# Kernel optimization log

Hardware: AMD Instinct MI355X
Metric: run time of the kernel (lower is better)

The kernel has to match this reference:

```python
import jax, jax.numpy as jnp
import numpy as np

B = 16; L_IN = 512; D_MODEL = 512; N_HEAD = 8; D_K = 128; D_V = 128
D_FF = 2048; N_LAYER = 4; WINDOW = (4, 4, 4); INNER = 5; COV = 4; NUM_SEQ = 128
N_LVL = len(WINDOW) + 1


def _build_mask_sizes():
    # Pyraformer get_mask: intra-scale band + inter-scale parent/child links.
    all_size = [L_IN]
    for w in WINDOW:
        all_size.append(all_size[-1] // w)
    L = sum(all_size)
    vis = np.zeros((L, L), dtype=bool)
    iw = INNER // 2
    starts = [0]
    for s in all_size:
        starts.append(starts[-1] + s)
    for li, sz in enumerate(all_size):
        s = starts[li]
        for i in range(s, s + sz):
            vis[i, max(i - iw, s):min(i + iw + 1, s + sz)] = True
    for li in range(1, len(all_size)):
        s = starts[li]
        for i in range(s, s + all_size[li]):
            l = (s - all_size[li - 1]) + (i - s) * WINDOW[li - 1]
            if i == s + all_size[li] - 1:
                r = s
            else:
                r = (s - all_size[li - 1]) + (i - s + 1) * WINDOW[li - 1]
            vis[i, l:r] = True
            vis[l:r, i] = True
    return ~vis, all_size  # True = blocked


def _build_indexes(all_size):
    # Pyraformer refer_points: for each fine position, its ancestor at each scale.
    idx = np.zeros((L_IN, len(all_size)), dtype=np.int64)
    for i in range(L_IN):
        idx[i, 0] = i
        former = i
        for j in range(1, len(all_size)):
            start = sum(all_size[:j])
            inner = former - (start - all_size[j - 1])
            former = start + min(inner // WINDOW[j - 1], all_size[j] - 1)
            idx[i, j] = former
    return idx


def _layer_norm(x, g, b, eps=1e-5):
    m = x.mean(-1, keepdims=True)
    v = x.var(-1, keepdims=True)
    return (x - m) / jnp.sqrt(v + eps) * g + b


def _conv1d(x, w, stride):  # x: [B,C,L], w: [O,I,K]
    return jax.lax.conv_general_dilated(x, w, (stride,), 'VALID',
                                        dimension_numbers=('NCH', 'OIH', 'NCH'))


def _forward(x, cov_w, cov_b, data_conv_w, down_w, down_b, conv_w, conv_b, bn_g, bn_b,
             up_w, up_b, bln_g, bln_b, wq, wk, wv, fc_w, ln1_g, ln1_b,
             ffn_w1, ffn_b1, ffn_w2, ffn_b2, ln2_g, ln2_b, attn_mask, gather_idx):
    Bsz = x.shape[0]
    # SingleStepEmbedding
    covs = jnp.concatenate([x[:, :, 1:1 + COV], (x[:, :, -1] / NUM_SEQ - 0.5)[..., None]], -1)
    cov_emb = covs @ cov_w + cov_b
    data = x[:, :, 0][:, None, :]                      # [B,1,L]
    data = jnp.concatenate([data[:, :, -1:], data, data[:, :, :1]], -1)  # circular pad k=3
    data_emb = _conv1d(data, data_conv_w, 1).transpose(0, 2, 1)          # [B,L,D]
    i = jnp.arange(D_MODEL)
    vec = jnp.power(10000.0, 2.0 * (i // 2) / D_MODEL)
    ang = jnp.arange(L_IN)[:, None] / vec
    pos_emb = jnp.where(i % 2 == 0, jnp.sin(ang), jnp.cos(ang))
    seq = cov_emb + data_emb + pos_emb[None]
    # Bottleneck_Construct (down -> strided convs -> up -> concat -> LN)
    tmp = (seq @ down_w + down_b).transpose(0, 2, 1)   # [B,d_k,L]
    outs = []
    for s in range(len(WINDOW)):
        tmp = _conv1d(tmp, conv_w[s], WINDOW[s]) + conv_b[s][None, :, None]
        mu = tmp.mean((0, 2), keepdims=True)
        var = tmp.var((0, 2), keepdims=True)
        tmp = (tmp - mu) / jnp.sqrt(var + 1e-5) * bn_g[s][None, :, None] + bn_b[s][None, :, None]
        tmp = jax.nn.elu(tmp)
        outs.append(tmp)
    pyr = jnp.concatenate(outs, axis=2).transpose(0, 2, 1) @ up_w + up_b
    enc = _layer_norm(jnp.concatenate([seq, pyr], axis=1), bln_g, bln_b)  # [B,Ltot,D]
    Lt = enc.shape[1]
    scale = np.float32(1.0 / np.sqrt(D_K))
    for l in range(N_LAYER):
        q = (enc @ wq[l]).reshape(Bsz, Lt, N_HEAD, D_K).transpose(0, 2, 1, 3)
        k = (enc @ wk[l]).reshape(Bsz, Lt, N_HEAD, D_K).transpose(0, 2, 1, 3)
        v = (enc @ wv[l]).reshape(Bsz, Lt, N_HEAD, D_V).transpose(0, 2, 1, 3)
        scores = jnp.einsum('bhqd,bhkd->bhqk', q, k) * scale
        scores = jnp.where(attn_mask[None, None], -1e9, scores)
        attn = jax.nn.softmax(scores, -1)
        o = jnp.einsum('bhqk,bhkd->bhqd', attn, v).transpose(0, 2, 1, 3).reshape(Bsz, Lt, N_HEAD * D_V)
        enc = _layer_norm(o @ fc_w[l] + enc, ln1_g[l], ln1_b[l])  # post-norm
        h = jax.nn.gelu(enc @ ffn_w1[l] + ffn_b1[l], approximate=False) @ ffn_w2[l] + ffn_b2[l]
        enc = _layer_norm(enc + h, ln2_g[l], ln2_b[l])
    # refer_points gather: [B, L_IN, N_LVL*D]
    out = enc[:, gather_idx.reshape(-1), :].reshape(Bsz, L_IN, N_LVL * D_MODEL)
    return out


def setup_inputs() -> dict:
    key = jax.random.key(0)
    ks = iter(jax.random.split(key, 64))

    def nrm(shape, scale=0.02):
        return (jax.random.normal(next(ks), shape) * scale).astype(jnp.float32)

    covs = jax.random.normal(next(ks), (B, L_IN, COV + 1), jnp.float32)
    ids = jax.random.randint(next(ks), (B, L_IN), 0, NUM_SEQ).astype(jnp.float32)
    x = jnp.concatenate([covs, ids[..., None]], -1)  # col0=data, 1..COV=covs, last=series id
    mask_np, all_size = _build_mask_sizes()
    idx = _build_indexes(all_size)
    nw = len(WINDOW)
    return dict(
        x=x,
        cov_w=nrm((COV + 1, D_MODEL)), cov_b=jnp.zeros((D_MODEL,), jnp.float32),
        data_conv_w=nrm((D_MODEL, 1, 3)),
        down_w=nrm((D_MODEL, D_K)), down_b=jnp.zeros((D_K,), jnp.float32),
        conv_w=nrm((nw, D_K, D_K, WINDOW[0])), conv_b=jnp.zeros((nw, D_K), jnp.float32),
        bn_g=jnp.ones((nw, D_K), jnp.float32), bn_b=jnp.zeros((nw, D_K), jnp.float32),
        up_w=nrm((D_K, D_MODEL)), up_b=jnp.zeros((D_MODEL,), jnp.float32),
        bln_g=jnp.ones((D_MODEL,), jnp.float32), bln_b=jnp.zeros((D_MODEL,), jnp.float32),
        wq=nrm((N_LAYER, D_MODEL, N_HEAD * D_K)), wk=nrm((N_LAYER, D_MODEL, N_HEAD * D_K)),
        wv=nrm((N_LAYER, D_MODEL, N_HEAD * D_V)), fc_w=nrm((N_LAYER, N_HEAD * D_V, D_MODEL)),
        ln1_g=jnp.ones((N_LAYER, D_MODEL), jnp.float32), ln1_b=jnp.zeros((N_LAYER, D_MODEL), jnp.float32),
        ffn_w1=nrm((N_LAYER, D_MODEL, D_FF)), ffn_b1=jnp.zeros((N_LAYER, D_FF), jnp.float32),
        ffn_w2=nrm((N_LAYER, D_FF, D_MODEL)), ffn_b2=jnp.zeros((N_LAYER, D_MODEL), jnp.float32),
        ln2_g=jnp.ones((N_LAYER, D_MODEL), jnp.float32), ln2_b=jnp.zeros((N_LAYER, D_MODEL), jnp.float32),
        attn_mask=jnp.asarray(mask_np),
        gather_idx=jnp.asarray(idx),
    )


def reference(x, cov_w, cov_b, data_conv_w, down_w, down_b, conv_w, conv_b, bn_g, bn_b,
              up_w, up_b, bln_g, bln_b, wq, wk, wv, fc_w, ln1_g, ln1_b,
              ffn_w1, ffn_b1, ffn_w2, ffn_b2, ln2_g, ln2_b, attn_mask, gather_idx):
    return _forward(x, cov_w, cov_b, data_conv_w, down_w, down_b, conv_w, conv_b, bn_g, bn_b,
                    up_w, up_b, bln_g, bln_b, wq, wk, wv, fc_w, ln1_g, ln1_b,
                    ffn_w1, ffn_b1, ffn_w2, ffn_b2, ln2_g, ln2_b, attn_mask, gather_idx)
```

## Files before the change

kernel.cpp:

```cpp
#include <hip/hip_runtime.h>
#include <math.h>

typedef unsigned short u16;
typedef unsigned int u32;
typedef __attribute__((ext_vector_type(8))) short s16x8;
typedef __attribute__((ext_vector_type(4))) float f32x4;
typedef __attribute__((ext_vector_type(4))) u32 u32x4;
typedef __attribute__((ext_vector_type(2))) u32 u32x2;

#define LT 680

static __device__ __forceinline__ float bf2f(u16 u) {
  u32 v = ((u32)u) << 16;
  return __builtin_bit_cast(float, v);
}
static __device__ __forceinline__ u16 f2bf(float f) {
  u32 u = __builtin_bit_cast(u32, f);
  u32 r = (u + 0x7FFFu + ((u >> 16) & 1u)) >> 16;
  return (u16)r;
}
static __device__ __forceinline__ float lo16(u32 u) {
  return __builtin_bit_cast(float, u << 16);
}
static __device__ __forceinline__ float hi16(u32 u) {
  return __builtin_bit_cast(float, u & 0xFFFF0000u);
}

static __device__ __forceinline__ void gload16(const u16* g, u16* l) {
  __builtin_amdgcn_global_load_lds(
      (const __attribute__((address_space(1))) u32*)g,
      (__attribute__((address_space(3))) u32*)l, 16, 0, 0);
}

__global__ void detect_k(const u32* __restrict__ blng, int* __restrict__ flag) {
  if (threadIdx.x == 0 && blockIdx.x == 0)
    *flag = (blng[0] == 0x3F803F80u) ? 1 : 0;
}

struct CvtArgs {
  const void* src[20];
  float* dst[20];
  int pre[21];
};

__global__ __launch_bounds__(256) void cvtall_k(CvtArgs a, const int* __restrict__ flag) {
  int i = blockIdx.x * 256 + threadIdx.x;
  if (i >= a.pre[20]) return;
  int s = 0;
#pragma unroll
  for (int k = 1; k <= 20; ++k)
    if (i >= a.pre[k]) s = k;
  int j = i - a.pre[s];
  bool isb = (*flag != 0);
  a.dst[s][j] = isb ? bf2f(((const u16*)a.src[s])[j]) : ((const float*)a.src[s])[j];
}

__global__ __launch_bounds__(256) void tc2_k(const void* __restrict__ S,
                                             u16* __restrict__ D, int K, int N,
                                             size_t sstride, size_t dstride,
                                             const int* __restrict__ flag) {
  __shared__ u16 t[32][33];
  size_t soff = (size_t)blockIdx.z * sstride;
  D += (size_t)blockIdx.z * dstride;
  int nb = blockIdx.x * 32, kb = blockIdx.y * 32;
  int lx = threadIdx.x & 31, ly = threadIdx.x >> 5;
  bool isb = (*flag != 0);
#pragma unroll
  for (int i = 0; i < 4; ++i) {
    size_t idx = soff + (size_t)(kb + ly + 8 * i) * N + nb + lx;
    t[ly + 8 * i][lx] = isb ? ((const u16*)S)[idx] : f2bf(((const float*)S)[idx]);
  }
  __syncthreads();
#pragma unroll
  for (int i = 0; i < 4; ++i)
    D[(size_t)(nb + ly + 8 * i) * K + kb + lx] = t[lx][ly + 8 * i];
}

static __device__ __forceinline__ void reduce2_256(float& a, float& b, float* sm) {
#pragma unroll
  for (int o = 32; o; o >>= 1) { a += __shfl_xor(a, o); b += __shfl_xor(b, o); }
  int w = threadIdx.x >> 6, ln = threadIdx.x & 63;
  if (ln == 0) { sm[w] = a; sm[4 + w] = b; }
  __syncthreads();
  a = sm[0] + sm[1] + sm[2] + sm[3];
  b = sm[4] + sm[5] + sm[6] + sm[7];
  __syncthreads();
}

__global__ __launch_bounds__(256) void emb_k(
    const float* __restrict__ x, const float* __restrict__ covw,
    const float* __restrict__ covb, const float* __restrict__ dw,
    float* __restrict__ seq) {
  int r = blockIdx.x;
  int b = r >> 9, l = r & 511;
  int base = r * 6;
  float c0 = x[base + 1], c1 = x[base + 2];
  float c2 = x[base + 3], c3 = x[base + 4];
  float c4 = x[base + 5] * 0.0078125f - 0.5f;
  int lm = (l + 511) & 511, lp = (l + 1) & 511;
  float dm = x[((b << 9) + lm) * 6];
  float d0 = x[base];
  float dp = x[((b << 9) + lp) * 6];
  for (int d = threadIdx.x; d < 512; d += 256) {
    float cov = c0 * covw[d] + c1 * covw[512 + d] +
                c2 * covw[1024 + d] + c3 * covw[1536 + d] +
                c4 * covw[2048 + d] + covb[d];
    float cv = dm * dw[d * 3] + d0 * dw[d * 3 + 1] + dp * dw[d * 3 + 2];
    float ex = (float)(2 * (d >> 1)) * (1.0f / 512.0f);
    float vec = powf(10000.0f, ex);
    float ang = (float)l / vec;
    float pos = (d & 1) ? cosf(ang) : sinf(ang);
    seq[((size_t)r << 9) + d] = cov + cv + pos;
  }
}

__global__ void tconv_k(const float* __restrict__ w, float* __restrict__ wt) {
  int e = blockIdx.x * 256 + threadIdx.x;
  if (e >= 3 * 512 * 128) return;
  int o = e & 127, ik = (e >> 7) & 511, s = e >> 16;
  wt[e] = w[s * 65536 + o * 512 + ik];
}

__global__ __launch_bounds__(256) void gemm_k(
    const float* __restrict__ A, const float* __restrict__ Bw,
    const float* __restrict__ bias, float* __restrict__ C,
    int M, int N, int K, int act) {
  __shared__ float As[16][64];
  __shared__ float Bs[16][64];
  int tid = threadIdx.x;
  int m0 = blockIdx.y * 64, n0 = blockIdx.x * 64;
  int tx = tid & 15, ty = tid >> 4;
  int la_r = tid >> 2, la_c = (tid & 3) << 2;
  int lb_r = tid >> 4, lb_c = (tid & 15) << 2;
  float acc[4][4] = {};
  for (int k0 = 0; k0 < K; k0 += 16) {
    float4 av = *reinterpret_cast<const float4*>(A + (size_t)(m0 + la_r) * K + k0 + la_c);
    As[la_c + 0][la_r] = av.x;
    As[la_c + 1][la_r] = av.y;
    As[la_c + 2][la_r] = av.z;
    As[la_c + 3][la_r] = av.w;
    float4 bv = *reinterpret_cast<const float4*>(Bw + (size_t)(k0 + lb_r) * N + n0 + lb_c);
    Bs[lb_r][lb_c + 0] = bv.x;
    Bs[lb_r][lb_c + 1] = bv.y;
    Bs[lb_r][lb_c + 2] = bv.z;
    Bs[lb_r][lb_c + 3] = bv.w;
    __syncthreads();
#pragma unroll
    for (int kk = 0; kk < 16; ++kk) {
      float4 a4 = *reinterpret_cast<const float4*>(&As[kk][ty << 2]);
      float4 b4 = *reinterpret_cast<const float4*>(&Bs[kk][tx << 2]);
      float ar[4] = {a4.x, a4.y, a4.z, a4.w};
      float br[4] = {b4.x, b4.y, b4.z, b4.w};
#pragma unroll
      for (int i = 0; i < 4; ++i)
#pragma unroll
        for (int j = 0; j < 4; ++j) acc[i][j] = fmaf(ar[i], br[j], acc[i][j]);
    }
    __syncthreads();
  }
  float bj[4] = {0.f, 0.f, 0.f, 0.f};
  if (bias) {
#pragma unroll
    for (int j = 0; j < 4; ++j) bj[j] = bias[n0 + (tx << 2) + j];
  }
#pragma unroll
  for (int i = 0; i < 4; ++i) {
    float4 o;
    float* op = reinterpret_cast<float*>(&o);
#pragma unroll
    for (int j = 0; j < 4; ++j) op[j] = acc[i][j] + bj[j];
    *reinterpret_cast<float4*>(C + (size_t)(m0 + (ty << 2) + i) * N + n0 + (tx << 2)) = o;
  }
}

static __device__ __forceinline__ f32x4 mfma16(s16x8 a, s16x8 b, f32x4 c) {
  return __builtin_amdgcn_mfma_f32_16x16x32_bf16(a, b, c, 0, 0, 0);
}

__global__ __launch_bounds__(256) void mgemm_k(
    const u16* __restrict__ A, const u16* __restrict__ BT,
    const float* __restrict__ bias, void* __restrict__ C,
    int M, int N, int K, int flags) {
  __shared__ char smem[49152];
  float* st = (float*)smem;
  int tid = threadIdx.x;

  int nN = N >> 7;
  int nwg = gridDim.x;
  int bid = blockIdx.x;
  int qq = nwg >> 3, rr = nwg & 7;
  int xcd = bid & 7, lin = bid >> 3;
  int s_ = (xcd < rr ? xcd * (qq + 1) : rr * (qq + 1) + (xcd - rr) * qq) + lin;
  int m0 = (s_ / nN) << 7, n0 = (s_ % nN) << 7;

  int l = tid & 63, wid = tid >> 6;
  int wr = wid >> 1, wc = wid & 1;
  f32x4 acc[4][4];
#pragma unroll
  for (int i = 0; i < 4; ++i)
#pragma unroll
    for (int j = 0; j < 4; ++j)
#pragma unroll
      for (int r = 0; r < 4; ++r) acc[i][j][r] = 0.f;

  int L8 = l >> 3;
  int p0_ = (l & 7) ^ L8;
  int rloc = 2 * L8 + (p0_ >> 2);
  int cel = (p0_ & 3) << 3;
  const u16* Ag0 = A + (size_t)m0 * K;
  const u16* Bg0 = BT + (size_t)n0 * K;

  auto STAGE = [&](int c, int kt) {
    u16* Ad = (u16*)smem + c * 8192;
    u16* Bd = Ad + 4096;
#pragma unroll
    for (int i = 0; i < 2; ++i) {
      int rg = wid * 32 + i * 16 + rloc;
      gload16(Ag0 + (size_t)rg * K + kt + cel, &Ad[(wid * 16 + i * 8) * 64]);
      gload16(Bg0 + (size_t)rg * K + kt + cel, &Bd[(wid * 16 + i * 8) * 64]);
    }
  };

  int sfrag = (((l & 1) << 2) + (l >> 4)) ^ (((l & 15) >> 1));
  int lhalf = (l & 15) >> 1;

  int nt = K >> 5;
  STAGE(0, 0);
  STAGE(1, 32);
  for (int t = 0; t < nt; ++t) {
    int cur = t % 3;
    if (t + 2 < nt) {
      STAGE((t + 2) % 3, (t + 2) << 5);
      asm volatile("s_waitcnt vmcnt(8)" ::: "memory");
    } else if (t + 1 < nt) {
      asm volatile("s_waitcnt vmcnt(4)" ::: "memory");
    } else {
      asm volatile("s_waitcnt vmcnt(0)" ::: "memory");
    }
    __builtin_amdgcn_s_barrier();
    const u16* Asb = (const u16*)smem + cur * 8192;
    const u16* Bsb = Asb + 4096;
    s16x8 af[4];
#pragma unroll
    for (int fr = 0; fr < 4; ++fr)
      af[fr] = *reinterpret_cast<const s16x8*>(
          &Asb[(wr * 32 + fr * 8 + lhalf) * 64 + sfrag * 8]);
#pragma unroll
    for (int fc = 0; fc < 4; ++fc) {
      s16x8 bf = *reinterpret_cast<const s16x8*>(
          &Bsb[(wc * 32 + fc * 8 + lhalf) * 64 + sfrag * 8]);
#pragma unroll
      for (int fr = 0; fr < 4; ++fr)
        acc[fr][fc] = mfma16(af[fr], bf, acc[fr][fc]);
    }
    asm volatile("s_waitcnt lgkmcnt(0)" ::: "memory");
    __builtin_amdgcn_s_barrier();
  }

  int cl = l & 15, rg2 = l >> 4;
  float bj[4];
#pragma unroll
  for (int fc = 0; fc < 4; ++fc)
    bj[fc] = bias ? bias[n0 + wc * 64 + fc * 16 + cl] : 0.f;
  int sr2 = tid >> 3;
  int scg = (tid & 7) << 4;
  int growb = m0 + ((sr2 >> 4) << 6) + (sr2 & 15);
#pragma unroll
  for (int fr = 0; fr < 4; ++fr) {
#pragma unroll
    for (int fc = 0; fc < 4; ++fc) {
      int col = wc * 64 + fc * 16 + cl;
#pragma unroll
      for (int r = 0; r < 4; ++r) {
        float v = acc[fr][fc][r] + bj[fc];
        if (flags & 2) {
          float zz = 1.5957691f * fmaf(0.044715f * v, v * v, v);
          v = v / (1.0f + __expf(-zz));
        }
        st[(wr * 16 + rg2 * 4 + r) * 132 + col] = v;
      }
    }
    __syncthreads();
    int gr = growb + fr * 16;
    if (flags & 1) {
      u32x4 o0, o1;
      u16* p0 = (u16*)&o0; u16* p1 = (u16*)&o1;
#pragma unroll
      for (int i = 0; i < 8; ++i) p0[i] = f2bf(st[sr2 * 132 + scg + i]);
#pragma unroll
      for (int i = 0; i < 8; ++i) p1[i] = f2bf(st[sr2 * 132 + scg + 8 + i]);
      u16* dst = (u16*)C + (size_t)gr * N + n0 + scg;
      __builtin_nontemporal_store(o0, reinterpret_cast<u32x4*>(dst));
      __builtin_nontemporal_store(o1, reinterpret_cast<u32x4*>(dst + 8));
    } else {
      float* dst = (float*)C + (size_t)gr * N + n0 + scg;
#pragma unroll
      for (int i = 0; i < 4; ++i)
        __builtin_nontemporal_store(
            *reinterpret_cast<const f32x4*>(&st[sr2 * 132 + scg + 4 * i]),
            reinterpret_cast<f32x4*>(dst + 4 * i));
    }
    __syncthreads();
  }
}

__global__ __launch_bounds__(256) void mg64_k(
    const u16* __restrict__ A, const u16* __restrict__ BT,
    const float* __restrict__ bias, float* __restrict__ C,
    int M, int N, int K) {
  __shared__ char smem[49152];
  float* st = (float*)smem;
  int tid = threadIdx.x;

  int nN = N >> 6;
  int nwg = gridDim.x;
  int bid = blockIdx.x;
  int qq = nwg >> 3, rr = nwg & 7;
  int xcd = bid & 7, lin = bid >> 3;
  int s_ = (xcd < rr ? xcd * (qq + 1) : rr * (qq + 1) + (xcd - rr) * qq) + lin;
  int m0 = (s_ / nN) << 6, n0 = (s_ % nN) << 6;

  int l = tid & 63, wid = tid >> 6;
  f32x4 acc[4];
#pragma unroll
  for (int j = 0; j < 4; ++j)
#pragma unroll
    for (int r = 0; r < 4; ++r) acc[j][r] = 0.f;

  int row8 = l >> 3, cp = l & 7;
  int cg = (cp ^ (row8 & 7)) << 3;
  const u16* Ag0 = A + (size_t)m0 * K;
  const u16* Bg0 = BT + (size_t)n0 * K;

  auto STAGE = [&](int c, int kt) {
    u16* Ad = (u16*)smem + c * 8192;
    u16* Bd = Ad + 4096;
#pragma unroll
    for (int i = 0; i < 2; ++i) {
      int r = wid * 16 + i * 8 + row8;
      gload16(Ag0 + (size_t)r * K + kt + cg, &Ad[(wid * 16 + i * 8) * 64]);
      gload16(Bg0 + (size_t)r * K + kt + cg, &Bd[(wid * 16 + i * 8) * 64]);
    }
  };

  int nt = K >> 6;
  STAGE(0, 0);
  STAGE(1, 64);
  for (int t = 0; t < nt; ++t) {
    int cur = t % 3;
    if (t + 2 < nt) {
      STAGE((t + 2) % 3, (t + 2) << 6);
      asm volatile("s_waitcnt vmcnt(8)" ::: "memory");
    } else if (t + 1 < nt) {
      asm volatile("s_waitcnt vmcnt(4)" ::: "memory");
    } else {
      asm volatile("s_waitcnt vmcnt(0)" ::: "memory");
    }
    __builtin_amdgcn_s_barrier();
    const u16* Asb = (const u16*)smem + cur * 8192;
    const u16* Bsb = Asb + 4096;
#pragma unroll
    for (int kk = 0; kk < 2; ++kk) {
      int kc = ((kk * 4 + (l >> 4)) ^ (l & 7)) * 8;
      s16x8 af = *reinterpret_cast<const s16x8*>(
          &Asb[(wid * 16 + (l & 15)) * 64 + kc]);
#pragma unroll
      for (int fc = 0; fc < 4; ++fc) {
        s16x8 bf = *reinterpret_cast<const s16x8*>(
            &Bsb[(fc * 16 + (l & 15)) * 64 + kc]);
        acc[fc] = mfma16(af, bf, acc[fc]);
      }
    }
    asm volatile("s_waitcnt lgkmcnt(0)" ::: "memory");
    __builtin_amdgcn_s_barrier();
  }

  int cl = l & 15, rg = l >> 4;
  float bj[4];
#pragma unroll
  for (int fc = 0; fc < 4; ++fc)
    bj[fc] = bias ? bias[n0 + fc * 16 + cl] : 0.f;
#pragma unroll
  for (int fc = 0; fc < 4; ++fc)
#pragma unroll
    for (int r = 0; r < 4; ++r)
      st[(wid * 16 + rg * 4 + r) * 80 + fc * 16 + cl] = acc[fc][r] + bj[fc];
  __syncthreads();
  int lr = tid >> 2;
  int lq = (tid & 3) << 2;
  float* dst = C + (size_t)(m0 + lr) * N + n0;
#pragma unroll
  for (int i = 0; i < 4; ++i)
    __builtin_nontemporal_store(
        *reinterpret_cast<const f32x4*>(&st[lr * 80 + lq + 16 * i]),
        reinterpret_cast<f32x4*>(dst + lq + 16 * i));
}

__global__ void im2col_k(const float* __restrict__ Y, float* __restrict__ X,
                         int Ti, int To) {
  int e = blockIdx.x * 256 + threadIdx.x;
  int ik = e & 511;
  int bt = e >> 9;
  int b = bt / To, t = bt - b * To;
  int i = ik >> 2, k = ik & 3;
  X[e] = Y[((size_t)(b * Ti + (t << 2) + k) << 7) + i];
}

__global__ __launch_bounds__(256) void bnelu_k(float* __restrict__ Y,
                                               const float* __restrict__ g,
                                               const float* __restrict__ be, int Ms) {
  __shared__ float sm[8];
  int ch = blockIdx.x;
  float s = 0.f, s2 = 0.f;
  for (int i = threadIdx.x; i < Ms; i += 256) {
    float v = Y[((size_t)i << 7) + ch];
    s += v; s2 += v * v;
  }
  reduce2_256(s, s2, sm);
  float mu = s / (float)Ms;
  float var = s2 / (float)Ms - mu * mu;
  float inv = rsqrtf(var + 1e-5f);
  float ga = g[ch], bb = be[ch];
  for (int i = threadIdx.x; i < Ms; i += 256) {
    float v = (Y[((size_t)i << 7) + ch] - mu) * inv * ga + bb;
    Y[((size_t)i << 7) + ch] = (v > 0.f) ? v : (expf(v) - 1.0f);
  }
}

__global__ void scat_k(const float* __restrict__ Y, float* __restrict__ cat,
                       int Ts, int off) {
  int e = blockIdx.x * 256 + threadIdx.x;
  int i = e & 127;
  int bt = e >> 7;
  int b = bt / Ts, t = bt - b * Ts;
  cat[((size_t)(b * 168 + off + t) << 7) + i] = Y[e];
}

__global__ __launch_bounds__(256) void catln_k(
    const float* __restrict__ seq, const float* __restrict__ pyr,
    const float* __restrict__ g, const float* __restrict__ be,
    float* __restrict__ out, u16* __restrict__ outb) {
  __shared__ float sm[8];
  int row = blockIdx.x;
  int b = row / LT, j = row - b * LT;
  const float* src = (j < 512) ? (seq + ((size_t)(b * 512 + j) << 9))
                               : (pyr + ((size_t)(b * 168 + j - 512) << 9));
  int t = threadIdx.x;
  float x0 = src[t], x1 = src[t + 256];
  float s = x0 + x1, s2 = x0 * x0 + x1 * x1;
  reduce2_256(s, s2, sm);
  float mu = s * 0.001953125f;
  float var = s2 * 0.001953125f - mu * mu;
  float inv = rsqrtf(var + 1e-5f);
  size_t ob = (size_t)row << 9;
  float v0 = (x0 - mu) * inv * g[t] + be[t];
  float v1 = (x1 - mu) * inv * g[t + 256] + be[t + 256];
  out[ob + t] = v0; out[ob + t + 256] = v1;
  outb[ob + t] = f2bf(v0); outb[ob + t + 256] = f2bf(v1);
}

__global__ __launch_bounds__(256) void lnres_k(
    const float* __restrict__ A, const float* __restrict__ R,
    const float* __restrict__ g, const float* __restrict__ be,
    float* __restrict__ O, u16* __restrict__ Ob) {
  __shared__ float sm[8];
  int row = blockIdx.x;
  size_t base = (size_t)row << 9;
  int t = threadIdx.x;
  float x0 = A[base + t] + R[base + t];
  float x1 = A[base + t + 256] + R[base + t + 256];
  float s = x0 + x1, s2 = x0 * x0 + x1 * x1;
  reduce2_256(s, s2, sm);
  float mu = s * 0.001953125f;
  float var = s2 * 0.001953125f - mu * mu;
  float inv = rsqrtf(var + 1e-5f);
  float v0 = (x0 - mu) * inv * g[t] + be[t];
  float v1 = (x1 - mu) * inv * g[t + 256] + be[t + 256];
  O[base + t] = v0; O[base + t + 256] = v1;
  Ob[base + t] = f2bf(v0); Ob[base + t + 256] = f2bf(v1);
}

__global__ __launch_bounds__(256) void attn_k(const u16* __restrict__ QKV,
                                              u16* __restrict__ O) {
  int cpx = gridDim.x >> 3;
  int bq = (blockIdx.x & 7) * cpx + (blockIdx.x >> 3);
  int b = bq / LT, q = bq - b * LT;
  int lane = threadIdx.x & 63, wv = threadIdx.x >> 6;
  int half = lane >> 5, t4 = (lane & 31) << 2;
  int h = (wv << 1) + half;
  int lvl = (q < 512) ? 0 : (q < 640) ? 1 : (q < 672) ? 2 : 3;
  int Sl = (lvl == 0) ? 0 : (lvl == 1) ? 512 : (lvl == 2) ? 640 : 672;
  int SZl = (lvl == 0) ? 512 : (lvl == 1) ? 128 : (lvl == 2) ? 32 : 8;
  int p = q - Sl;
  int Sc = (lvl == 1) ? 0 : (lvl == 2) ? 512 : 640;
  int Sp = (lvl == 0) ? 512 : (lvl == 1) ? 640 : 672;
  int tg[10];
  bool vd[10];
#pragma unroll
  for (int jj = 0; jj < 10; ++jj) {
    int tgt; bool valid;
    if (jj < 5) { int pp = p - 2 + jj; valid = (pp >= 0 && pp < SZl); tgt = Sl + pp; }
    else if (jj < 9) { valid = (lvl > 0); tgt = Sc + p * 4 + (jj - 5); }
    else { valid = (lvl < 3); tgt = Sp + (p >> 2); }
    if (!valid) tgt = q;
    tg[jj] = tgt; vd[jj] = valid;
  }
  size_t hoff = h * 128 + t4;
  u32x2 qv = *reinterpret_cast<const u32x2*>(QKV + (size_t)bq * 3072 + hoff);
  float q0 = lo16(qv.x), q1 = hi16(qv.x), q2 = lo16(qv.y), q3 = hi16(qv.y);
  size_t base3 = (size_t)b * LT;
  float sc[10];
  float mx = -1e30f;
#pragma unroll
  for (int jj = 0; jj < 10; ++jj) {
    u32x2 kv = *reinterpret_cast<const u32x2*>(
        QKV + (base3 + tg[jj]) * 3072 + 1024 + hoff);
    float pr = q0 * lo16(kv.x) + q1 * hi16(kv.x) + q2 * lo16(kv.y) + q3 * hi16(kv.y);
#pragma unroll
    for (int o = 16; o; o >>= 1) pr += __shfl_xor(pr, o);
    float sv = vd[jj] ? pr * 0.08838834764831845f : -1e30f;
    sc[jj] = sv;
    mx = fmaxf(mx, sv);
  }
  float den = 0.f;
#pragma unroll
  for (int jj = 0; jj < 10; ++jj) { sc[jj] = expf(sc[jj] - mx); den += sc[jj]; }
  float invd = 1.0f / den;
  float o0 = 0.f, o1 = 0.f, o2 = 0.f, o3 = 0.f;
#pragma unroll
  for (int jj = 0; jj < 10; ++jj) {
    u32x2 vv = *reinterpret_cast<const u32x2*>(
        QKV + (base3 + tg[jj]) * 3072 + 2048 + hoff);
    float w = sc[jj] * invd;
    o0 = fmaf(w, lo16(vv.x), o0);
    o1 = fmaf(w, hi16(vv.x), o1);
    o2 = fmaf(w, lo16(vv.y), o2);
    o3 = fmaf(w, hi16(vv.y), o3);
  }
  u32x2 ov;
  ov.x = (u32)f2bf(o0) | ((u32)f2bf(o1) << 16);
  ov.y = (u32)f2bf(o2) | ((u32)f2bf(o3) << 16);
  *reinterpret_cast<u32x2*>(O + (size_t)bq * 1024 + hoff) = ov;
}

__global__ void gather_k(const float* __restrict__ enc, void* __restrict__ out,
                         const int* __restrict__ flag) {
  int e = blockIdx.x * 256 + threadIdx.x;
  int d = e & 511;
  int lvl = (e >> 9) & 3;
  int i = (e >> 11) & 511;
  int b = e >> 20;
  int g = (lvl == 0) ? i
        : (lvl == 1) ? (512 + (i >> 2))
        : (lvl == 2) ? (640 + (i >> 4))
                     : (672 + (i >> 6));
  float v = enc[(((size_t)b * LT + g) << 9) + d];
  if (*flag) ((u16*)out)[e] = f2bf(v);
  else       ((float*)out)[e] = v;
}

extern "C" void kernel_launch(void* const* d_in, const int* in_sizes, int n_in,
                              void* d_out, int out_size, void* d_ws, size_t ws_size,
                              hipStream_t stream) {
  float* ws = (float*)d_ws;
  size_t off = 0;
  auto alloc = [&](size_t n) { float* p = ws + off; off += (n + 63) & ~(size_t)63; return p; };

  int* flag = (int*)alloc(64);

  static const int cvt_n[26] = {
      49152, 2560, 512, 1536, 65536, 128, 196608, 384, 384, 384,
      65536, 512, 512, 512, 2097152, 2097152, 2097152, 2097152, 2048, 2048,
      4194304, 8192, 4194304, 2048, 2048, 2048};
  float* cf[26];
  for (int i = 0; i < 26; ++i) cf[i] = alloc(cvt_n[i]);

  float* cwt     = alloc(196608);
  float* enc     = alloc((size_t)10880 * 512);
  float* tmp     = alloc((size_t)10880 * 512);
  u16*   encb    = (u16*)alloc((size_t)10880 * 512 / 2);
  u16*   qkv     = (u16*)alloc((size_t)10880 * 3072 / 2);
  u16*   attnout = (u16*)alloc((size_t)10880 * 1024 / 2);
  u16*   qkvw    = (u16*)alloc((size_t)4 * 3072 * 512 / 2);
  u16*   fcT     = (u16*)alloc((size_t)4 * 512 * 1024 / 2);
  u16*   w1T     = (u16*)alloc((size_t)4 * 2048 * 512 / 2);
  u16*   w2T     = (u16*)alloc((size_t)4 * 512 * 2048 / 2);
  u16*   H1      = qkv;

  float* seq   = (float*)qkv;
  float* pyr   = seq + 4194304;
  float* tdown = pyr + 1376256;
  float* xcol  = tdown + 1048576;
  float* ya    = xcol + 1048576;
  float* yb    = ya + 262144;
  float* yc    = yb + 65536;
  float* cat   = yc + 16384;

  detect_k<<<1, 64, 0, stream>>>((const u32*)d_in[12], flag);
  {
    static const int segs[20] = {0,1,2,3,4,5,6,7,8,9,10,11,12,13,18,19,21,23,24,25};
    CvtArgs a;
    int acc_ = 0;
    for (int k = 0; k < 20; ++k) {
      int i = segs[k];
      a.src[k] = d_in[i];
      a.dst[k] = cf[i];
      a.pre[k] = acc_;
      acc_ += cvt_n[i];
    }
    a.pre[20] = acc_;
    cvtall_k<<<(acc_ + 255) / 256, 256, 0, stream>>>(a, flag);
  }

  const float *x = cf[0], *covw = cf[1], *covb = cf[2], *dconvw = cf[3],
              *downw = cf[4], *downb = cf[5], *convw = cf[6], *convb = cf[7],
              *bng = cf[8], *bnb = cf[9], *upw = cf[10], *upb = cf[11],
              *blng = cf[12], *blnb = cf[13], *ln1g = cf[18], *ln1b = cf[19],
              *b1 = cf[21], *b2 = cf[23], *ln2g = cf[24], *ln2b = cf[25];

  tc2_k<<<dim3(32, 16, 4), 256, 0, stream>>>(d_in[14], qkvw,           512, 1024, 524288, 1572864, flag);
  tc2_k<<<dim3(32, 16, 4), 256, 0, stream>>>(d_in[15], qkvw + 524288,  512, 1024, 524288, 1572864, flag);
  tc2_k<<<dim3(32, 16, 4), 256, 0, stream>>>(d_in[16], qkvw + 1048576, 512, 1024, 524288, 1572864, flag);
  tc2_k<<<dim3(16, 32, 4), 256, 0, stream>>>(d_in[17], fcT,  1024, 512, 524288, 524288, flag);
  tc2_k<<<dim3(64, 16, 4), 256, 0, stream>>>(d_in[20], w1T,  512, 2048, 1048576, 1048576, flag);
  tc2_k<<<dim3(16, 64, 4), 256, 0, stream>>>(d_in[22], w2T,  2048, 512, 1048576, 1048576, flag);

  emb_k<<<8192, 256, 0, stream>>>(x, covw, covb, dconvw, seq);
  tconv_k<<<(3 * 512 * 128 + 255) / 256, 256, 0, stream>>>(convw, cwt);

  gemm_k<<<dim3(2, 128), 256, 0, stream>>>(seq, downw, downb, tdown, 8192, 128, 512, 0);
  im2col_k<<<(16 * 128 * 512) / 256, 256, 0, stream>>>(tdown, xcol, 512, 128);
  gemm_k<<<dim3(2, 32), 256, 0, stream>>>(xcol, cwt, convb, ya, 2048, 128, 512, 0);
  bnelu_k<<<128, 256, 0, stream>>>(ya, bng, bnb, 2048);
  scat_k<<<(2048 * 128) / 256, 256, 0, stream>>>(ya, cat, 128, 0);
  im2col_k<<<(16 * 32 * 512) / 256, 256, 0, stream>>>(ya, xcol, 128, 32);
  gemm_k<<<dim3(2, 8), 256, 0, stream>>>(xcol, cwt + 65536, convb + 128, yb, 512, 128, 512, 0);
  bnelu_k<<<128, 256, 0, stream>>>(yb, bng + 128, bnb + 128, 512);
  scat_k<<<(512 * 128) / 256, 256, 0, stream>>>(yb, cat, 32, 128);
  im2col_k<<<(16 * 8 * 512) / 256, 256, 0, stream>>>(yb, xcol, 32, 8);
  gemm_k<<<dim3(2, 2), 256, 0, stream>>>(xcol, cwt + 131072, convb + 256, yc, 128, 128, 512, 0);
  bnelu_k<<<128, 256, 0, stream>>>(yc, bng + 256, bnb + 256, 128);
  scat_k<<<(128 * 128) / 256, 256, 0, stream>>>(yc, cat, 8, 160);
  gemm_k<<<dim3(8, 42), 256, 0, stream>>>(cat, upw, upb, pyr, 2688, 512, 128, 0);
  catln_k<<<10880, 256, 0, stream>>>(seq, pyr, blng, blnb, enc, encb);

  for (int l = 0; l < 4; ++l) {
    const u16* qw  = qkvw + (size_t)l * 3072 * 512;
    const u16* fw  = fcT + (size_t)l * 524288;
    const u16* w1w = w1T + (size_t)l * 1048576;
    const u16* w2w = w2T + (size_t)l * 1048576;
    mgemm_k<<<85 * 24, 256, 0, stream>>>(encb, qw, nullptr, qkv, 10880, 3072, 512, 1);
    attn_k<<<16 * LT, 256, 0, stream>>>(qkv, attnout);
    mg64_k<<<170 * 8, 256, 0, stream>>>(attnout, fw, nullptr, tmp, 10880, 512, 1024);
    lnres_k<<<10880, 256, 0, stream>>>(tmp, enc, ln1g + l * 512, ln1b + l * 512, enc, encb);
    mgemm_k<<<85 * 16, 256, 0, stream>>>(encb, w1w, b1 + l * 2048, H1, 10880, 2048, 512, 3);
    mg64_k<<<170 * 8, 256, 0, stream>>>(H1, w2w, b2 + l * 512, tmp, 10880, 512, 2048);
    lnres_k<<<10880, 256, 0, stream>>>(tmp, enc, ln2g + l * 512, ln2b + l * 512, enc, encb);
  }

  gather_k<<<(16 * 512 * 2048) / 256, 256, 0, stream>>>(enc, d_out, flag);
}
```

Baseline: 1.228 ms.

## Split-K the N=512 output-projection GEMMs and fuse partial sums into layernorm

The fc and FFN-down GEMMs (N=512, K=1024/2048) now run as split-K with two halves, doubling the workgroup count to 2720 so the GPU is better occupied. Each half writes fp32 partials to a separate buffer, and the residual layernorm kernel sums both partials plus the bias. In exchange, each GEMM writes twice as much fp32 output and the layernorm reads one extra activation-sized tensor. Some unused converted-weight buffers are also dropped from the workspace to make room.

```diff
diff --git a/kernel.cpp b/kernel.cpp
--- a/kernel.cpp
+++ b/kernel.cpp
@@ -304,17 +304,20 @@
   }
 }
 
-__global__ __launch_bounds__(256) void mg64_k(
+__global__ __launch_bounds__(256) void mg64sk_k(
     const u16* __restrict__ A, const u16* __restrict__ BT,
-    const float* __restrict__ bias, float* __restrict__ C,
-    int M, int N, int K) {
+    float* __restrict__ C, int M, int N, int K, int Ksub) {
   __shared__ char smem[49152];
   float* st = (float*)smem;
   int tid = threadIdx.x;
 
+  int half = blockIdx.x & 1;
+  int bid = blockIdx.x >> 1;
+  int koff = half * Ksub;
+  C += (size_t)half * M * N;
+
   int nN = N >> 6;
-  int nwg = gridDim.x;
-  int bid = blockIdx.x;
+  int nwg = gridDim.x >> 1;
   int qq = nwg >> 3, rr = nwg & 7;
   int xcd = bid & 7, lin = bid >> 3;
   int s_ = (xcd < rr ? xcd * (qq + 1) : rr * (qq + 1) + (xcd - rr) * qq) + lin;
@@ -329,8 +332,8 @@
 
   int row8 = l >> 3, cp = l & 7;
   int cg = (cp ^ (row8 & 7)) << 3;
-  const u16* Ag0 = A + (size_t)m0 * K;
-  const u16* Bg0 = BT + (size_t)n0 * K;
+  const u16* Ag0 = A + (size_t)m0 * K + koff;
+  const u16* Bg0 = BT + (size_t)n0 * K + koff;
 
   auto STAGE = [&](int c, int kt) {
     u16* Ad = (u16*)smem + c * 8192;
@@ -343,7 +346,7 @@
     }
   };
 
-  int nt = K >> 6;
+  int nt = Ksub >> 6;
   STAGE(0, 0);
   STAGE(1, 64);
   for (int t = 0; t < nt; ++t) {
@@ -376,15 +379,11 @@
   }
 
   int cl = l & 15, rg = l >> 4;
-  float bj[4];
 #pragma unroll
   for (int fc = 0; fc < 4; ++fc)
-    bj[fc] = bias ? bias[n0 + fc * 16 + cl] : 0.f;
-#pragma unroll
-  for (int fc = 0; fc < 4; ++fc)
 #pragma unroll
     for (int r = 0; r < 4; ++r)
-      st[(wid * 16 + rg * 4 + r) * 80 + fc * 16 + cl] = acc[fc][r] + bj[fc];
+      st[(wid * 16 + rg * 4 + r) * 80 + fc * 16 + cl] = acc[fc][r];
   __syncthreads();
   int lr = tid >> 2;
   int lq = (tid & 3) << 2;
@@ -459,16 +458,19 @@
   outb[ob + t] = f2bf(v0); outb[ob + t + 256] = f2bf(v1);
 }
 
-__global__ __launch_bounds__(256) void lnres_k(
-    const float* __restrict__ A, const float* __restrict__ R,
+__global__ __launch_bounds__(256) void lnres3_k(
+    const float* __restrict__ A0, const float* __restrict__ A1,
+    const float* __restrict__ bias, const float* __restrict__ R,
     const float* __restrict__ g, const float* __restrict__ be,
     float* __restrict__ O, u16* __restrict__ Ob) {
   __shared__ float sm[8];
   int row = blockIdx.x;
   size_t base = (size_t)row << 9;
   int t = threadIdx.x;
-  float x0 = A[base + t] + R[base + t];
-  float x1 = A[base + t + 256] + R[base + t + 256];
+  float b0 = bias ? bias[t] : 0.f;
+  float b1 = bias ? bias[t + 256] : 0.f;
+  float x0 = A0[base + t] + A1[base + t] + b0 + R[base + t];
+  float x1 = A0[base + t + 256] + A1[base + t + 256] + b1 + R[base + t + 256];
   float s = x0 + x1, s2 = x0 * x0 + x1 * x1;
   reduce2_256(s, s2, sm);
   float mu = s * 0.001953125f;
@@ -573,11 +575,17 @@
       65536, 512, 512, 512, 2097152, 2097152, 2097152, 2097152, 2048, 2048,
       4194304, 8192, 4194304, 2048, 2048, 2048};
   float* cf[26];
-  for (int i = 0; i < 26; ++i) cf[i] = alloc(cvt_n[i]);
+  for (int i = 0; i < 26; ++i) {
+    if (i == 14 || i == 15 || i == 16 || i == 17 || i == 20 || i == 22) {
+      cf[i] = nullptr;
+      continue;
+    }
+    cf[i] = alloc(cvt_n[i]);
+  }
 
   float* cwt     = alloc(196608);
   float* enc     = alloc((size_t)10880 * 512);
-  float* tmp     = alloc((size_t)10880 * 512);
+  float* tmpsk   = alloc((size_t)2 * 10880 * 512);
   u16*   encb    = (u16*)alloc((size_t)10880 * 512 / 2);
   u16*   qkv     = (u16*)alloc((size_t)10880 * 3072 / 2);
   u16*   attnout = (u16*)alloc((size_t)10880 * 1024 / 2);
@@ -651,11 +659,13 @@
     const u16* w2w = w2T + (size_t)l * 1048576;
     mgemm_k<<<85 * 24, 256, 0, stream>>>(encb, qw, nullptr, qkv, 10880, 3072, 512, 1);
     attn_k<<<16 * LT, 256, 0, stream>>>(qkv, attnout);
-    mg64_k<<<170 * 8, 256, 0, stream>>>(attnout, fw, nullptr, tmp, 10880, 512, 1024);
-    lnres_k<<<10880, 256, 0, stream>>>(tmp, enc, ln1g + l * 512, ln1b + l * 512, enc, encb);
+    mg64sk_k<<<2 * 170 * 8, 256, 0, stream>>>(attnout, fw, tmpsk, 10880, 512, 1024, 512);
+    lnres3_k<<<10880, 256, 0, stream>>>(tmpsk, tmpsk + (size_t)10880 * 512, nullptr,
+                                        enc, ln1g + l * 512, ln1b + l * 512, enc, encb);
     mgemm_k<<<85 * 16, 256, 0, stream>>>(encb, w1w, b1 + l * 2048, H1, 10880, 2048, 512, 3);
-    mg64_k<<<170 * 8, 256, 0, stream>>>(H1, w2w, b2 + l * 512, tmp, 10880, 512, 2048);
-    lnres_k<<<10880, 256, 0, stream>>>(tmp, enc, ln2g + l * 512, ln2b + l * 512, enc, encb);
+    mg64sk_k<<<2 * 170 * 8, 256, 0, stream>>>(H1, w2w, tmpsk, 10880, 512, 2048, 1024);
+    lnres3_k<<<10880, 256, 0, stream>>>(tmpsk, tmpsk + (size_t)10880 * 512, b2 + l * 512,
+                                        enc, ln2g + l * 512, ln2b + l * 512, enc, encb);
   }
 
   gather_k<<<(16 * 512 * 2048) / 256, 256, 0, stream>>>(enc, d_out, flag);
```

Measured after the change: 1.269 ms. 3.4% more time.
